# Kernel optimization log

Hardware: AMD Instinct MI355X
Metric: run time of the kernel (lower is better)

The kernel has to match this reference:

```python
import jax, jax.numpy as jnp
import numpy as np

EMBED = 256
HEADS = 8
HEAD_DIM = EMBED // HEADS  # 32
B, L = 2, 4096
END_X = END_Y = 64
THETA = 10000.0


def _axial_rope_tables(dim, end_x, end_y, theta):
    # dim = per-head dim (32); dim//4 = 8 freqs per axis -> 16 complex pairs
    freqs = 1.0 / theta ** (np.arange(0, dim, 4)[: dim // 4].astype(np.float32) / dim)
    t = np.arange(end_x * end_y, dtype=np.float32)
    t_x = t % end_x
    t_y = np.floor(t / end_x)
    ang_x = np.outer(t_x, freqs)  # [L, dim//4]
    ang_y = np.outer(t_y, freqs)
    ang = np.concatenate([ang_x, ang_y], axis=-1)  # [L, dim//2]
    return jnp.asarray(np.cos(ang)), jnp.asarray(np.sin(ang))

ROPE_COS, ROPE_SIN = _axial_rope_tables(HEAD_DIM, END_X, END_Y, THETA)


def _apply_rope(x, cos, sin):
    # x: [B, H, L, D]; interpret consecutive pairs as complex numbers
    b, h, l, d = x.shape
    xr = x.reshape(b, h, l, d // 2, 2)
    real, imag = xr[..., 0], xr[..., 1]
    c = cos[None, None, :, :]  # [1,1,L,D/2]
    s = sin[None, None, :, :]
    out_r = real * c - imag * s
    out_i = real * s + imag * c
    return jnp.stack([out_r, out_i], axis=-1).reshape(b, h, l, d)


def setup_inputs() -> dict:
    key = jax.random.key(0)
    ks = jax.random.split(key, 11)
    sw = 1.0 / np.sqrt(EMBED)
    inp = {
        'q': jax.random.normal(ks[0], (B, L, EMBED), jnp.float32),
        'k': jax.random.normal(ks[1], (B, L, EMBED), jnp.float32),
        'v': jax.random.normal(ks[2], (B, L, EMBED), jnp.float32),
        'Wq': jax.random.normal(ks[3], (EMBED, EMBED), jnp.float32) * sw,
        'bq': jnp.zeros((EMBED,), jnp.float32),
        'Wk': jax.random.normal(ks[4], (EMBED, EMBED), jnp.float32) * sw,
        'bk': jnp.zeros((EMBED,), jnp.float32),
        'Wv': jax.random.normal(ks[5], (EMBED, EMBED), jnp.float32) * sw,
        'bv': jnp.zeros((EMBED,), jnp.float32),
        'Wo': jax.random.normal(ks[6], (EMBED, EMBED), jnp.float32) * sw,
        'bo': jnp.zeros((EMBED,), jnp.float32),
    }
    return inp


def reference(q, k, v, Wq, bq, Wk, bk, Wv, bv, Wo, bo):
    b, l, _ = q.shape
    # QKV projections (torch Linear: x @ W.T + b)
    qp = q @ Wq.T + bq
    kp = k @ Wk.T + bk
    vp = v @ Wv.T + bv
    # separate heads -> [B, H, L, D]
    sep = lambda x: x.reshape(b, l, HEADS, HEAD_DIM).transpose(0, 2, 1, 3)
    qh, kh, vh = sep(qp), sep(kp), sep(vp)
    # rotary position encoding (fp32, complex pair multiply)
    qh = _apply_rope(qh, ROPE_COS, ROPE_SIN)
    kh = _apply_rope(kh, ROPE_COS, ROPE_SIN)
    # scaled dot-product attention
    scale = 1.0 / np.sqrt(HEAD_DIM)
    scores = jnp.einsum('bhqd,bhkd->bhqk', qh, kh) * scale
    attn = jax.nn.softmax(scores, axis=-1)
    out = jnp.einsum('bhqk,bhkd->bhqd', attn, vh)
    # recombine heads and output projection
    out = out.transpose(0, 2, 1, 3).reshape(b, l, EMBED)
    return out @ Wo.T + bo
```

## Files before the change

### kernel.cpp

```cpp
#include <hip/hip_runtime.h>

#define SEQ   4096
#define EMBED 256
#define HEADS 8
#define HDIM  32
#define BH    16
#define NROW  8192

typedef __bf16 bf16;
typedef bf16  bf16x8 __attribute__((ext_vector_type(8)));
typedef bf16  bf16x4 __attribute__((ext_vector_type(4)));
typedef float f32x4  __attribute__((ext_vector_type(4)));

static __device__ __forceinline__ bf16x4 cvt4(float4 v) {
  bf16x4 r;
  r.x = (bf16)v.x; r.y = (bf16)v.y; r.z = (bf16)v.z; r.w = (bf16)v.w;
  return r;
}

static __device__ __forceinline__ float fast_exp2(float x) {
  float r;
  asm volatile("v_exp_f32 %0, %1" : "=v"(r) : "v"(x));
  return r;
}

__global__ __launch_bounds__(256, 4) void proj_kernel(
    const float* __restrict__ qx, const float* __restrict__ kx, const float* __restrict__ vx,
    const float* __restrict__ Wq, const float* __restrict__ bq,
    const float* __restrict__ Wk, const float* __restrict__ bk,
    const float* __restrict__ Wv, const float* __restrict__ bv,
    bf16* __restrict__ qh, bf16* __restrict__ kh, bf16* __restrict__ vt,
    float qscale)
{
  __shared__ alignas(16) bf16 As[2][64][72];
  __shared__ alignas(16) bf16 Bs[2][64][72];
  const int z = blockIdx.z;
  const float* X    = (z == 0) ? qx : (z == 1) ? kx : vx;
  const float* W    = (z == 0) ? Wq : (z == 1) ? Wk : Wv;
  const float* bias = (z == 0) ? bq : (z == 1) ? bk : bv;

  const int tid  = threadIdx.x;
  const int wave = tid >> 6;
  const int lane = tid & 63;
  const int quad = lane >> 4;
  const int l16  = lane & 15;
  const int row0 = blockIdx.x * 64;
  const int col0 = blockIdx.y * 64;

  const int sr = tid >> 4;
  const int sc = (tid & 15) * 4;

  f32x4 acc[4] = { {0.f,0.f,0.f,0.f},{0.f,0.f,0.f,0.f},
                   {0.f,0.f,0.f,0.f},{0.f,0.f,0.f,0.f} };

#pragma unroll
  for (int p = 0; p < 4; ++p) {
    int r = p * 16 + sr;
    float4 av = *(const float4*)&X[(size_t)(row0 + r) * EMBED + sc];
    *(bf16x4*)&As[0][r][sc] = cvt4(av);
    float4 wv = *(const float4*)&W[(size_t)(col0 + r) * EMBED + sc];
    *(bf16x4*)&Bs[0][r][sc] = cvt4(wv);
  }
  __syncthreads();

#pragma unroll
  for (int it = 0; it < 4; ++it) {
    const int cur = it & 1;

    float4 pav[4], pwv[4];
    if (it < 3) {
      const int kn = (it + 1) * 64;
#pragma unroll
      for (int p = 0; p < 4; ++p) {
        int r = p * 16 + sr;
        pav[p] = *(const float4*)&X[(size_t)(row0 + r) * EMBED + kn + sc];
        pwv[p] = *(const float4*)&W[(size_t)(col0 + r) * EMBED + kn + sc];
      }
    }

#pragma unroll
    for (int kk = 0; kk < 2; ++kk) {
      bf16x8 a = *(const bf16x8*)&As[cur][wave * 16 + l16][kk * 32 + quad * 8];
#pragma unroll
      for (int nt = 0; nt < 4; ++nt) {
        bf16x8 b = *(const bf16x8*)&Bs[cur][nt * 16 + l16][kk * 32 + quad * 8];
        acc[nt] = __builtin_amdgcn_mfma_f32_16x16x32_bf16(a, b, acc[nt], 0, 0, 0);
      }
    }

    if (it < 3) {
#pragma unroll
      for (int p = 0; p < 4; ++p) {
        int r = p * 16 + sr;
        *(bf16x4*)&As[cur ^ 1][r][sc] = cvt4(pav[p]);
        *(bf16x4*)&Bs[cur ^ 1][r][sc] = cvt4(pwv[p]);
      }
      __syncthreads();
    }
  }

  if (z < 2) {
    bf16* dst = z ? kh : qh;
    const float out_scale = z ? 1.0f : qscale;
#pragma unroll
    for (int nt = 0; nt < 4; ++nt) {
#pragma unroll
      for (int r = 0; r < 4; ++r) {
        int row = row0 + wave * 16 + quad * 4 + r;
        int col = col0 + nt * 16 + l16;
        float val = acc[nt][r] + bias[col];
        int l = row & (SEQ - 1);
        {
          float other = __shfl_xor(val, 1);
          int d = col & (HDIM - 1);
          int j = d >> 1;
          float fr = exp2f(-1.6609640474436813f * (float)(j & 7));
          float t  = (j < 8) ? (float)(l & 63) : (float)(l >> 6);
          float ang = t * fr;
          float sv, cv;
          __sincosf(ang, &sv, &cv);
          val = (col & 1) ? (other * sv + val * cv) : (val * cv - other * sv);
        }
        val *= out_scale;
        int b = row >> 12;
        int h = col >> 5;
        int d = col & (HDIM - 1);
        dst[((size_t)((b * HEADS + h) * SEQ + l)) * HDIM + d] = (bf16)val;
      }
    }
  } else {
    __syncthreads();
#pragma unroll
    for (int nt = 0; nt < 4; ++nt) {
      float bcol = bias[col0 + nt * 16 + l16];
      bf16x4 pk;
      pk.x = (bf16)(acc[nt][0] + bcol);
      pk.y = (bf16)(acc[nt][1] + bcol);
      pk.z = (bf16)(acc[nt][2] + bcol);
      pk.w = (bf16)(acc[nt][3] + bcol);
      *(bf16x4*)&As[0][nt * 16 + l16][wave * 16 + quad * 4] = pk;
    }
    __syncthreads();
    const int e   = tid >> 2;
    const int seg = tid & 3;
    const int ge  = col0 + e;
    const int hh  = ge >> 5;
    const int d   = ge & (HDIM - 1);
    const int bidx = row0 >> 12;
    const int l0   = row0 & (SEQ - 1);
    size_t dstbase = ((size_t)(bidx * HEADS + hh) * HDIM + d) * SEQ + l0 + seg * 16;
    bf16x8 t0 = *(const bf16x8*)&As[0][e][seg * 16];
    bf16x8 t1 = *(const bf16x8*)&As[0][e][seg * 16 + 8];
    *(bf16x8*)&vt[dstbase]     = t0;
    *(bf16x8*)&vt[dstbase + 8] = t1;
  }
}

__global__ __launch_bounds__(512, 4) void attn_kernel(
    const bf16* __restrict__ Q, const bf16* __restrict__ K,
    const bf16* __restrict__ Vt, bf16* __restrict__ H)
{
  __shared__ alignas(16) bf16 Ks[2][4][64][8];
  __shared__ alignas(16) bf16 Vs[2][4][64][8];
  __shared__ alignas(16) bf16 Pa[8][16][72];

  const int tid  = threadIdx.x;
  const int wave = tid >> 6;
  const int lane = tid & 63;
  const int quad = lane >> 4;
  const int l16  = lane & 15;

  const int id = blockIdx.x;
  const int bh = ((id & 7) << 1) | (id >> 8);
  const int q0 = ((id >> 3) & 31) * 128 + wave * 16;

  const bf16* Qg = Q  + (size_t)bh * SEQ * HDIM;
  const bf16* Kg = K  + (size_t)bh * SEQ * HDIM;
  const bf16* Vg = Vt + (size_t)bh * HDIM * SEQ;

  bf16x8 qf = *(const bf16x8*)&Qg[(size_t)(q0 + l16) * HDIM + quad * 8];

  f32x4 o0 = {0.f,0.f,0.f,0.f};
  f32x4 o1 = {0.f,0.f,0.f,0.f};
  float lsum = 0.f;

  const bool isK = tid < 256;
  const int  tt  = tid & 255;
  const bf16* sbase;
  size_t sstep;
  bf16* d0;
  if (isK) {
    const int r  = tt >> 2;
    const int qq = tt & 3;
    sbase = Kg + (size_t)r * HDIM + qq * 8;
    sstep = (size_t)64 * HDIM;
    d0 = &Ks[0][r >> 4][qq * 16 + (r & 15)][0];
  } else {
    const int d  = tt >> 3;
    const int sg = tt & 7;
    sbase = Vg + (size_t)d * SEQ + sg * 8;
    sstep = 64;
    d0 = &Vs[0][((d >> 4) << 1) | (sg >> 2)][(sg & 3) * 16 + (d & 15)][0];
  }
  bf16* d1 = d0 + 4 * 64 * 8;

  const f32x4 minit = {-12.f,-12.f,-12.f,-12.f};

  *(bf16x8*)d0 = *(const bf16x8*)sbase;
  __syncthreads();

  for (int t = 0; t < 64; ++t) {
    const int cur = t & 1;
    const int tn  = (t < 63) ? t + 1 : 63;
    bf16x8 g = *(const bf16x8*)&sbase[(size_t)tn * sstep];

    const bf16* KT = &Ks[cur][0][0][0];
    const bf16* VT = &Vs[cur][0][0][0];

    bf16x8 kf0 = *(const bf16x8*)&KT[(0 * 64 + lane) * 8];
    bf16x8 kf1 = *(const bf16x8*)&KT[(1 * 64 + lane) * 8];
    bf16x8 kf2 = *(const bf16x8*)&KT[(2 * 64 + lane) * 8];
    bf16x8 kf3 = *(const bf16x8*)&KT[(3 * 64 + lane) * 8];

    f32x4 s[4];
    s[0] = __builtin_amdgcn_mfma_f32_16x16x32_bf16(kf0, qf, minit, 0, 0, 0);
    s[1] = __builtin_amdgcn_mfma_f32_16x16x32_bf16(kf1, qf, minit, 0, 0, 0);
    s[2] = __builtin_amdgcn_mfma_f32_16x16x32_bf16(kf2, qf, minit, 0, 0, 0);
    s[3] = __builtin_amdgcn_mfma_f32_16x16x32_bf16(kf3, qf, minit, 0, 0, 0);

    bf16x8 vf0 = *(const bf16x8*)&VT[(0 * 64 + lane) * 8];
    bf16x8 vf1 = *(const bf16x8*)&VT[(1 * 64 + lane) * 8];
    bf16x8 vf2 = *(const bf16x8*)&VT[(2 * 64 + lane) * 8];
    bf16x8 vf3 = *(const bf16x8*)&VT[(3 * 64 + lane) * 8];

#pragma unroll
    for (int nt = 0; nt < 4; ++nt) {
      float p0 = fast_exp2(s[nt][0]);
      float p1 = fast_exp2(s[nt][1]);
      float p2 = fast_exp2(s[nt][2]);
      float p3 = fast_exp2(s[nt][3]);
      lsum += (p0 + p1) + (p2 + p3);
      bf16x4 pk;
      pk.x = (bf16)p0; pk.y = (bf16)p1; pk.z = (bf16)p2; pk.w = (bf16)p3;
      *(bf16x4*)&Pa[wave][l16][nt * 16 + quad * 4] = pk;
    }

    asm volatile("s_waitcnt lgkmcnt(0)" ::: "memory");

    bf16x8 pf0 = *(const bf16x8*)&Pa[wave][l16][quad * 8];
    bf16x8 pf1 = *(const bf16x8*)&Pa[wave][l16][32 + quad * 8];
    o0 = __builtin_amdgcn_mfma_f32_16x16x32_bf16(pf0, vf0, o0, 0, 0, 0);
    o0 = __builtin_amdgcn_mfma_f32_16x16x32_bf16(pf1, vf1, o0, 0, 0, 0);
    o1 = __builtin_amdgcn_mfma_f32_16x16x32_bf16(pf0, vf2, o1, 0, 0, 0);
    o1 = __builtin_amdgcn_mfma_f32_16x16x32_bf16(pf1, vf3, o1, 0, 0, 0);

    *(bf16x8*)(cur ? d0 : d1) = g;
    __syncthreads();
  }

  lsum += __shfl_xor(lsum, 16);
  lsum += __shfl_xor(lsum, 32);

  const int b = bh >> 3;
  const int h = bh & 7;
#pragma unroll
  for (int r = 0; r < 4; ++r) {
    float tot  = __shfl(lsum, quad * 4 + r);
    float invr = 1.0f / tot;
    int   qg   = q0 + quad * 4 + r;
    size_t base = ((size_t)(b * SEQ + qg)) * EMBED + h * HDIM;
    H[base + l16]      = (bf16)(o0[r] * invr);
    H[base + 16 + l16] = (bf16)(o1[r] * invr);
  }
}

__global__ __launch_bounds__(256) void out_proj_kernel(
    const bf16* __restrict__ Hm, const float* __restrict__ W,
    const float* __restrict__ bias, float* __restrict__ out)
{
  __shared__ alignas(16) bf16 As[64][72];
  __shared__ alignas(16) bf16 Bs[64][72];
  const int tid  = threadIdx.x;
  const int wave = tid >> 6;
  const int lane = tid & 63;
  const int quad = lane >> 4;
  const int l16  = lane & 15;
  const int row0 = blockIdx.x * 64;
  const int col0 = blockIdx.y * 64;

  f32x4 acc[4] = { {0.f,0.f,0.f,0.f},{0.f,0.f,0.f,0.f},
                   {0.f,0.f,0.f,0.f},{0.f,0.f,0.f,0.f} };

  for (int k0 = 0; k0 < EMBED; k0 += 64) {
#pragma unroll
    for (int p = 0; p < 2; ++p) {
      int f = p * 256 + tid;
      int r = f >> 3;
      int c = (f & 7) * 8;
      *(bf16x8*)&As[r][c] = *(const bf16x8*)&Hm[(size_t)(row0 + r) * EMBED + k0 + c];
    }
#pragma unroll
    for (int p = 0; p < 4; ++p) {
      int f = p * 256 + tid;
      int r = f >> 4;
      int c = (f & 15) * 4;
      float4 wv = *(const float4*)&W[(size_t)(col0 + r) * EMBED + k0 + c];
      *(bf16x4*)&Bs[r][c] = cvt4(wv);
    }
    __syncthreads();
#pragma unroll
    for (int kk = 0; kk < 2; ++kk) {
      bf16x8 a = *(const bf16x8*)&As[wave * 16 + l16][kk * 32 + quad * 8];
#pragma unroll
      for (int nt = 0; nt < 4; ++nt) {
        bf16x8 b = *(const bf16x8*)&Bs[nt * 16 + l16][kk * 32 + quad * 8];
        acc[nt] = __builtin_amdgcn_mfma_f32_16x16x32_bf16(a, b, acc[nt], 0, 0, 0);
      }
    }
    __syncthreads();
  }

#pragma unroll
  for (int nt = 0; nt < 4; ++nt) {
#pragma unroll
    for (int r = 0; r < 4; ++r) {
      int row = row0 + wave * 16 + quad * 4 + r;
      int col = col0 + nt * 16 + l16;
      out[(size_t)row * EMBED + col] = acc[nt][r] + bias[col];
    }
  }
}

extern "C" void kernel_launch(void* const* d_in, const int* in_sizes, int n_in,
                              void* d_out, int out_size, void* d_ws, size_t ws_size,
                              hipStream_t stream) {
  (void)in_sizes; (void)n_in; (void)out_size; (void)ws_size;
  const float* q  = (const float*)d_in[0];
  const float* k  = (const float*)d_in[1];
  const float* v  = (const float*)d_in[2];
  const float* Wq = (const float*)d_in[3];
  const float* bq = (const float*)d_in[4];
  const float* Wk = (const float*)d_in[5];
  const float* bk = (const float*)d_in[6];
  const float* Wv = (const float*)d_in[7];
  const float* bv = (const float*)d_in[8];
  const float* Wo = (const float*)d_in[9];
  const float* bo = (const float*)d_in[10];
  float* out = (float*)d_out;

  const size_t headElems = (size_t)BH * SEQ * HDIM;
  bf16* qh = (bf16*)d_ws;
  bf16* kh = qh + headElems;
  bf16* vt = kh + headElems;
  bf16* Hm = vt + headElems;

  const float qs = 0.2550436604f;

  proj_kernel<<<dim3(128, 4, 3), dim3(256), 0, stream>>>(q, k, v, Wq, bq, Wk, bk,
                                                         Wv, bv, qh, kh, vt, qs);
  attn_kernel<<<dim3(512), dim3(512), 0, stream>>>(qh, kh, vt, Hm);
  out_proj_kernel<<<dim3(128, 4), dim3(256), 0, stream>>>(Hm, Wo, bo, out);
}
```

Before: 168.9 us.

## Double-buffer LDS tiles in output projection with register prefetch

```diff
diff --git a/kernel.cpp b/kernel.cpp
--- a/kernel.cpp
+++ b/kernel.cpp
@@ -274,12 +274,12 @@
   }
 }
 
-__global__ __launch_bounds__(256) void out_proj_kernel(
+__global__ __launch_bounds__(256, 4) void out_proj_kernel(
     const bf16* __restrict__ Hm, const float* __restrict__ W,
     const float* __restrict__ bias, float* __restrict__ out)
 {
-  __shared__ alignas(16) bf16 As[64][72];
-  __shared__ alignas(16) bf16 Bs[64][72];
+  __shared__ alignas(16) bf16 As[2][64][72];
+  __shared__ alignas(16) bf16 Bs[2][64][72];
   const int tid  = threadIdx.x;
   const int wave = tid >> 6;
   const int lane = tid & 63;
@@ -288,36 +288,70 @@
   const int row0 = blockIdx.x * 64;
   const int col0 = blockIdx.y * 64;
 
+  const int ar = tid >> 3;
+  const int ac = (tid & 7) * 8;
+  const int br = tid >> 4;
+  const int bc = (tid & 15) * 4;
+
   f32x4 acc[4] = { {0.f,0.f,0.f,0.f},{0.f,0.f,0.f,0.f},
                    {0.f,0.f,0.f,0.f},{0.f,0.f,0.f,0.f} };
 
-  for (int k0 = 0; k0 < EMBED; k0 += 64) {
-#pragma unroll
-    for (int p = 0; p < 2; ++p) {
-      int f = p * 256 + tid;
-      int r = f >> 3;
-      int c = (f & 7) * 8;
-      *(bf16x8*)&As[r][c] = *(const bf16x8*)&Hm[(size_t)(row0 + r) * EMBED + k0 + c];
-    }
-#pragma unroll
-    for (int p = 0; p < 4; ++p) {
-      int f = p * 256 + tid;
-      int r = f >> 4;
-      int c = (f & 15) * 4;
-      float4 wv = *(const float4*)&W[(size_t)(col0 + r) * EMBED + k0 + c];
-      *(bf16x4*)&Bs[r][c] = cvt4(wv);
-    }
-    __syncthreads();
+#pragma unroll
+  for (int p = 0; p < 2; ++p) {
+    int r = p * 32 + ar;
+    *(bf16x8*)&As[0][r][ac] = *(const bf16x8*)&Hm[(size_t)(row0 + r) * EMBED + ac];
+  }
+#pragma unroll
+  for (int p = 0; p < 4; ++p) {
+    int r = p * 16 + br;
+    float4 wv = *(const float4*)&W[(size_t)(col0 + r) * EMBED + bc];
+    *(bf16x4*)&Bs[0][r][bc] = cvt4(wv);
+  }
+  __syncthreads();
+
+#pragma unroll
+  for (int it = 0; it < 4; ++it) {
+    const int cur = it & 1;
+
+    bf16x8 pa[2];
+    float4 pw[4];
+    if (it < 3) {
+      const int kn = (it + 1) * 64;
+#pragma unroll
+      for (int p = 0; p < 2; ++p) {
+        int r = p * 32 + ar;
+        pa[p] = *(const bf16x8*)&Hm[(size_t)(row0 + r) * EMBED + kn + ac];
+      }
+#pragma unroll
+      for (int p = 0; p < 4; ++p) {
+        int r = p * 16 + br;
+        pw[p] = *(const float4*)&W[(size_t)(col0 + r) * EMBED + kn + bc];
+      }
+    }
+
 #pragma unroll
     for (int kk = 0; kk < 2; ++kk) {
-      bf16x8 a = *(const bf16x8*)&As[wave * 16 + l16][kk * 32 + quad * 8];
+      bf16x8 a = *(const bf16x8*)&As[cur][wave * 16 + l16][kk * 32 + quad * 8];
 #pragma unroll
       for (int nt = 0; nt < 4; ++nt) {
-        bf16x8 b = *(const bf16x8*)&Bs[nt * 16 + l16][kk * 32 + quad * 8];
+        bf16x8 b = *(const bf16x8*)&Bs[cur][nt * 16 + l16][kk * 32 + quad * 8];
         acc[nt] = __builtin_amdgcn_mfma_f32_16x16x32_bf16(a, b, acc[nt], 0, 0, 0);
       }
     }
-    __syncthreads();
+
+    if (it < 3) {
+#pragma unroll
+      for (int p = 0; p < 2; ++p) {
+        int r = p * 32 + ar;
+        *(bf16x8*)&As[cur ^ 1][r][ac] = pa[p];
+      }
+#pragma unroll
+      for (int p = 0; p < 4; ++p) {
+        int r = p * 16 + br;
+        *(bf16x4*)&Bs[cur ^ 1][r][bc] = cvt4(pw[p]);
+      }
+      __syncthreads();
+    }
   }
 
 #pragma unroll
```

Measured after the change: 167.5 us. About the same (-0.8%).
